# Optimization experiments

Measured on AMD Instinct MI355X. Metric: run time of the kernel, lower is better.

## Reference

```python
import jax, jax.numpy as jnp
import numpy as np

B, T, HID = 1, 2048, 1024
H, D = 16, 64
S = 64            # selection_block_size / sliding window / compress block
MAXK = 8          # max_selected_blocks
W_ENT, W_SP = 0.01, 0.01
NB = T // S       # 32 blocks (T divisible by S -> no padding branch)


def setup_inputs() -> dict:
    key = jax.random.key(0)
    ks = jax.random.split(key, 8)
    rn = lambda k, shp, s=0.02: jax.random.normal(k, shp, jnp.float32) * s
    return {
        'hidden_states': rn(ks[0], (B, T, HID), 1.0),
        'Wq': rn(ks[1], (HID, H * D)),
        'Wk': rn(ks[2], (HID, H * D)),
        'Wv': rn(ks[3], (HID, H * D)),
        'Wo': rn(ks[4], (H * D, HID)),
        'Wc': rn(ks[5], (S * D, D)),      # shared k/v compress MLP (same module in torch)
        'bc': jnp.zeros((D,), jnp.float32),
        'k_scale': jnp.ones((1,), jnp.float32),
        'k_bias': jnp.zeros((1,), jnp.float32),
        'Ws': rn(ks[6], (HID, 3 * H)),
        'bs': jnp.zeros((3 * H,), jnp.float32),
    }


def _local_attn(q, k, v):
    # lucidrains LocalAttention: window S, causal, look_backward=1, scale d^-0.5
    b, h, t, d = q.shape
    nw = t // S
    qw = q.reshape(b, h, nw, S, d)
    kw = k.reshape(b, h, nw, S, d)
    vw = v.reshape(b, h, nw, S, d)
    k_prev = jnp.concatenate([jnp.zeros_like(kw[:, :, :1]), kw[:, :, :-1]], axis=2)
    v_prev = jnp.concatenate([jnp.zeros_like(vw[:, :, :1]), vw[:, :, :-1]], axis=2)
    kc = jnp.concatenate([k_prev, kw], axis=3)   # (b,h,nw,2S,d)
    vc = jnp.concatenate([v_prev, vw], axis=3)
    scores = jnp.einsum('bhwid,bhwjd->bhwij', qw, kc) / jnp.sqrt(jnp.float32(d))
    qpos = jnp.arange(S)[:, None]
    krel = jnp.arange(2 * S)[None, :] - S        # key pos relative to window start
    wins = jnp.arange(nw)[:, None, None]
    allowed = (krel <= qpos)[None] & (wins * S + krel[None] >= 0)  # (nw,S,2S)
    NEG = -jnp.finfo(scores.dtype).max
    scores = jnp.where(allowed[None, None], scores, NEG)
    p = jax.nn.softmax(scores, axis=-1)
    return jnp.einsum('bhwij,bhwjd->bhwid', p, vc).reshape(b, h, t, d)


def reference(hidden_states, Wq, Wk, Wv, Wo, Wc, bc, k_scale, k_bias, Ws, bs):
    x = hidden_states
    scale = 1.0 / jnp.sqrt(jnp.float32(D))
    q = (x @ Wq).reshape(B, T, H, D).transpose(0, 2, 1, 3)
    k = (x @ Wk).reshape(B, T, H, D).transpose(0, 2, 1, 3)
    v = (x @ Wv).reshape(B, T, H, D).transpose(0, 2, 1, 3)

    sliding_out = _local_attn(q, k, v)

    # block compression (shared MLP for k and v, exact-erf GELU as in torch)
    k_blk = k.reshape(B, H, NB, S * D)
    v_blk = v.reshape(B, H, NB, S * D)
    kc = jax.nn.gelu(k_blk @ Wc + bc, approximate=False)   # (B,H,NB,D)
    vc = jax.nn.gelu(v_blk @ Wc + bc, approximate=False)

    importance = jnp.einsum('bhid,bhjd->bhij', q, kc) * scale   # (B,H,T,NB)
    comp_probs = jax.nn.softmax(importance, axis=-1)
    comp_out = jnp.einsum('bhij,bhjd->bhid', comp_probs, vc)

    # per-query-block scores, entropy-driven dynamic k
    block_scores = importance.reshape(B, H, NB, S, NB).mean(axis=3)   # (B,H,NB,NB)
    block_probs = jax.nn.softmax(block_scores, axis=-1)
    entropy = -jnp.sum(block_probs * jnp.log(block_probs + 1e-9), axis=-1)
    max_entropy = jnp.log(jnp.float32(NB))
    norm_ent = entropy / (max_entropy + 1e-9)
    k_ratio = jax.nn.sigmoid(k_scale[0] * norm_ent + k_bias[0])
    dynamic_k = jnp.clip(MAXK * k_ratio, 1.0, float(MAXK)).astype(jnp.int32)  # torch .long() truncates
    avg_k = dynamic_k.astype(jnp.float32).mean()

    _, topk_idx = jax.lax.top_k(block_scores, MAXK)                 # (B,H,NB,MAXK)
    k_mask = jnp.arange(MAXK)[None, None, None, :] < dynamic_k[..., None]
    sel = (topk_idx[..., None] == jnp.arange(NB)) & k_mask[..., None]
    mask = sel.any(axis=-2)                                         # (B,H,NB,NB)
    mask = mask | jnp.eye(NB, dtype=bool)[None, None]
    sparse_mask = jnp.repeat(jnp.repeat(mask, S, axis=2), S, axis=3)  # (B,H,T,T)

    attn = jnp.einsum('bhid,bhjd->bhij', q, k) * scale
    NEG = -jnp.finfo(attn.dtype).max
    attn = jnp.where(sparse_mask, attn, NEG)
    fine_probs = jax.nn.softmax(attn, axis=-1)
    fine_out = jnp.einsum('bhij,bhjd->bhid', fine_probs, v)

    strategy = jax.nn.sigmoid(x @ Ws + bs).reshape(B, T, H, 3).transpose(0, 2, 1, 3)  # (B,H,T,3)
    combined = jnp.stack([sliding_out, comp_out, fine_out], axis=-1)  # (B,H,T,D,3)
    out = jnp.einsum('bhnds,bhns->bhnd', combined, strategy)
    merged = out.transpose(0, 2, 1, 3).reshape(B, T, H * D)
    output = merged @ Wo

    entropy_loss = jnp.mean((k_ratio - norm_ent) ** 2)
    aux_loss = W_ENT * entropy_loss + W_SP * k_ratio.mean()
    return output, avg_k, aux_loss
```

## Files before the change

kernel.cpp:

```cpp
#include <hip/hip_runtime.h>
#include <math.h>
#include <stdint.h>

typedef unsigned short u16;
typedef short v8s __attribute__((ext_vector_type(8)));
typedef float v4f __attribute__((ext_vector_type(4)));

constexpr int kT   = 2048;
constexpr int kHID = 1024;
constexpr int kH   = 16;
constexpr int kNB  = 32;
constexpr size_t MB = 1ull << 20;

__device__ __forceinline__ float b2f(u16 u) { unsigned x = ((unsigned)u) << 16; return __uint_as_float(x); }
__device__ __forceinline__ u16 f2b(float f) {
  unsigned x = __float_as_uint(f);
  x += 0x7FFFu + ((x >> 16) & 1u);
  return (u16)(x >> 16);
}
__device__ __forceinline__ v4f mfma16(v8s a, v8s b, v4f c) {
  return __builtin_amdgcn_mfma_f32_16x16x32_bf16(a, b, c, 0, 0, 0);
}
__device__ __forceinline__ void gl_lds16(const void* g, void* l) {
  __builtin_amdgcn_global_load_lds((const __attribute__((address_space(1))) uint32_t*)g,
                                   (__attribute__((address_space(3))) uint32_t*)l, 16, 0, 0);
}

__global__ __launch_bounds__(256) void prep_kernel(
    const float* __restrict__ x, const float* __restrict__ Wq, const float* __restrict__ Wk,
    const float* __restrict__ Wv, const float* __restrict__ Wo, const float* __restrict__ Wc,
    const float* __restrict__ Wsp,
    u16* __restrict__ xh,
    u16* __restrict__ WqtH, u16* __restrict__ WktH,
    u16* __restrict__ WvtH, u16* __restrict__ WotH, u16* __restrict__ WctH, u16* __restrict__ WctL,
    u16* __restrict__ Wst) {
  __shared__ float tbuf[32][33];
  int bid = blockIdx.x;
  const int tid = threadIdx.x;
  if (bid < 1024) {
    int i = bid * 2048 + tid * 8;
    float4 a = *(const float4*)(x + i), b = *(const float4*)(x + i + 4);
    float tv[8] = {a.x, a.y, a.z, a.w, b.x, b.y, b.z, b.w};
    union { u16 s[8]; uint4 u; } hs;
#pragma unroll
    for (int e = 0; e < 8; ++e) hs.s[e] = f2b(tv[e]);
    *(uint4*)(xh + i) = hs.u;
    return;
  }
  bid -= 1024;
  const float* W; u16* Hh; u16* Ll; int Kd, Nd, bx, by;
  if (bid < 4096) {
    int wsel = bid >> 10, sub = bid & 1023;
    W  = wsel == 0 ? Wq : wsel == 1 ? Wk : wsel == 2 ? Wv : Wo;
    Hh = wsel == 0 ? WqtH : wsel == 1 ? WktH : wsel == 2 ? WvtH : WotH;
    Ll = nullptr;
    Kd = 1024; Nd = 1024;
    bx = (sub & 31) * 32; by = (sub >> 5) * 32;
  } else if (bid < 4096 + 256) {
    int sub = bid - 4096;
    W = Wc; Hh = WctH; Ll = WctL;
    Kd = 4096; Nd = 64;
    bx = (sub & 1) * 32; by = (sub >> 1) * 32;
  } else {
    int i = (bid - 4096 - 256) * 256 + tid;
    int n = i >> 10, k2 = i & 1023;
    float v = (n < 48) ? Wsp[(size_t)k2 * 48 + n] : 0.f;
    Wst[(size_t)n * 1024 + k2] = f2b(v);
    return;
  }
  const int lx = tid & 31, ly = tid >> 5;
  for (int i2 = ly; i2 < 32; i2 += 8) tbuf[i2][lx] = W[(size_t)(by + i2) * Nd + bx + lx];
  __syncthreads();
  for (int i2 = ly; i2 < 32; i2 += 8) {
    float xv = tbuf[lx][i2];
    size_t idx = (size_t)(bx + i2) * Kd + by + lx;
    u16 h = f2b(xv);
    Hh[idx] = h;
    if (Ll) Ll[idx] = f2b(xv - b2f(h));
  }
}

__global__ __launch_bounds__(256) void proj_gemm(const u16* __restrict__ xh,
                                                 const u16* __restrict__ WkH, const u16* __restrict__ WqH,
                                                 const u16* __restrict__ WvH, const u16* __restrict__ Wst,
                                                 const float* __restrict__ bsp,
                                                 u16* __restrict__ kbf, u16* __restrict__ qh,
                                                 u16* __restrict__ vbf, float* __restrict__ strat) {
  __shared__ u16 AsH[64 * 64], BsH[128 * 64];
  const int b = blockIdx.x;
  const int slot = (b & 7) * 100 + (b >> 3);
  const int panel = slot >> 5, bmi = slot & 31;
  int z, bni;
  if (panel < 8)       { z = 0; bni = panel; }
  else if (panel < 16) { z = 1; bni = panel - 8; }
  else if (panel < 24) { z = 2; bni = panel - 16; }
  else                 { z = 3; bni = 0; }
  const int bm = bmi * 64, bn = bni * 128;
  const u16* Bh = (z == 0) ? WkH : (z == 1) ? WqH : (z == 2) ? WvH : Wst;
  const int tid = threadIdx.x, w = tid >> 6, lane = tid & 63;
  const int lg = lane >> 4, l16 = lane & 15;
  const int wr = w >> 1, wc = w & 1;
  v4f acc[2][4] = {};
  for (int k0 = 0; k0 < kHID; k0 += 64) {
    __syncthreads();
#pragma unroll
    for (int p = 0; p < 2; ++p) {
      int s = tid + p * 256, row = s >> 3, sf = (s & 7) ^ (row & 7);
      gl_lds16(xh + (size_t)(bm + row) * kHID + k0 + sf * 8, (char*)AsH + s * 16);
    }
#pragma unroll
    for (int p = 0; p < 4; ++p) {
      int s = tid + p * 256, row = s >> 3, sf = (s & 7) ^ (row & 7);
      gl_lds16(Bh + (size_t)(bn + row) * kHID + k0 + sf * 8, (char*)BsH + s * 16);
    }
    __syncthreads();
#pragma unroll
    for (int kk = 0; kk < 2; ++kk) {
      v8s bh4[4];
#pragma unroll
      for (int j = 0; j < 4; ++j) {
        int col = wc * 64 + j * 16 + l16;
        bh4[j] = *(const v8s*)((const char*)BsH + col * 128 + (((kk * 4 + lg) ^ (col & 7)) * 16));
      }
#pragma unroll
      for (int i = 0; i < 2; ++i) {
        int row = wr * 32 + i * 16 + l16;
        v8s ah = *(const v8s*)((const char*)AsH + row * 128 + (((kk * 4 + lg) ^ (row & 7)) * 16));
#pragma unroll
        for (int j = 0; j < 4; ++j) acc[i][j] = mfma16(ah, bh4[j], acc[i][j]);
      }
    }
  }
#pragma unroll
  for (int i = 0; i < 2; ++i)
#pragma unroll
    for (int j = 0; j < 4; ++j)
#pragma unroll
      for (int r = 0; r < 4; ++r) {
        int row = bm + wr * 32 + i * 16 + lg * 4 + r;
        int col = bn + wc * 64 + j * 16 + l16;
        float val = acc[i][j][r];
        if (z == 3) {
          if (col < 48) strat[(size_t)row * 48 + col] = 1.f / (1.f + expf(-(val + bsp[col])));
        } else {
          u16 hh = f2b(val);
          size_t idx = (size_t)row * kHID + col;
          if (z == 0) kbf[idx] = hh;
          else if (z == 1) qh[idx] = hh;
          else vbf[idx] = hh;
        }
      }
}

__global__ __launch_bounds__(256) void cgemm_fused(const u16* __restrict__ kbf,
                                                   const u16* __restrict__ vbf,
                                                   const u16* __restrict__ WcH, const u16* __restrict__ WcL,
                                                   float* __restrict__ Pk, float* __restrict__ Pv) {
  __shared__ u16 AsH[64 * 64], BsH[64 * 64], BsL[64 * 64];
  const int bm = blockIdx.y * 64;
  const int isK = (blockIdx.z < 8);
  const int ks = isK ? blockIdx.z : blockIdx.z - 8;
  const u16* Asrc = isK ? kbf : vbf;
  float* P = isK ? Pk : Pv;
  const int tid = threadIdx.x;
  const int w = tid >> 6, lane = tid & 63;
  const int lg = lane >> 4, l16 = lane & 15;
  const int wr = w >> 1, wc = w & 1;
  v4f acc[2][2] = {};
  for (int k0 = ks * 512; k0 < ks * 512 + 512; k0 += 64) {
    __syncthreads();
#pragma unroll
    for (int ss = 0; ss < 2; ++ss) {
      int s = tid + ss * 256, row = s >> 3, sf = (s & 7) ^ (row & 7);
      int r = bm + row;
      size_t abase = ((size_t)((r & 31) * 64 + (k0 >> 6))) * kHID + (r >> 5) * 64 + sf * 8;
      gl_lds16(Asrc + abase, (char*)AsH + s * 16);
      gl_lds16(WcH + (size_t)row * 4096 + k0 + sf * 8, (char*)BsH + s * 16);
      if (isK) gl_lds16(WcL + (size_t)row * 4096 + k0 + sf * 8, (char*)BsL + s * 16);
    }
    __syncthreads();
    v8s ah[2][2], bh[2][2];
#pragma unroll
    for (int i = 0; i < 2; ++i)
#pragma unroll
      for (int kk = 0; kk < 2; ++kk) {
        int row = wr * 32 + i * 16 + l16;
        ah[i][kk] = *(const v8s*)((const char*)AsH + row * 128 + (((kk * 4 + lg) ^ (row & 7)) * 16));
        int col = wc * 32 + i * 16 + l16;
        bh[i][kk] = *(const v8s*)((const char*)BsH + col * 128 + (((kk * 4 + lg) ^ (col & 7)) * 16));
      }
#pragma unroll
    for (int i = 0; i < 2; ++i)
#pragma unroll
      for (int j = 0; j < 2; ++j) {
        acc[i][j] = mfma16(ah[i][0], bh[j][0], acc[i][j]);
        acc[i][j] = mfma16(ah[i][1], bh[j][1], acc[i][j]);
      }
    if (isK) {
      v8s bl[2][2];
#pragma unroll
      for (int i = 0; i < 2; ++i)
#pragma unroll
        for (int kk = 0; kk < 2; ++kk) {
          int col = wc * 32 + i * 16 + l16;
          bl[i][kk] = *(const v8s*)((const char*)BsL + col * 128 + (((kk * 4 + lg) ^ (col & 7)) * 16));
        }
#pragma unroll
      for (int i = 0; i < 2; ++i)
#pragma unroll
        for (int j = 0; j < 2; ++j) {
          acc[i][j] = mfma16(ah[i][0], bl[j][0], acc[i][j]);
          acc[i][j] = mfma16(ah[i][1], bl[j][1], acc[i][j]);
        }
    }
  }
#pragma unroll
  for (int i = 0; i < 2; ++i)
#pragma unroll
    for (int j = 0; j < 2; ++j)
#pragma unroll
      for (int r = 0; r < 4; ++r) {
        int row = bm + wr * 32 + i * 16 + lg * 4 + r;
        int col = wc * 32 + j * 16 + l16;
        P[(size_t)ks * 32768 + (size_t)row * 64 + col] = acc[i][j][r];
      }
}

__global__ __launch_bounds__(256) void attn_fused(const u16* __restrict__ qh,
                                                  const u16* __restrict__ kb_,
                                                  const u16* __restrict__ vb_,
                                                  const float* __restrict__ Pk,
                                                  const float* __restrict__ Pv,
                                                  const float* __restrict__ bc,
                                                  const float* __restrict__ strat,
                                                  const float* __restrict__ kscale_p,
                                                  const float* __restrict__ kbias_p,
                                                  float* __restrict__ krb,
                                                  float* __restrict__ neb,
                                                  int* __restrict__ dkb,
                                                  u16* __restrict__ merged) {
  __shared__ char smem[40960] __attribute__((aligned(128)));
  const int b = blockIdx.x;
  const int xcd = b & 7, slot = b >> 3;
  const int h = xcd + 8 * (slot >> 5);
  const int qb = slot & 31;
  const int tid = threadIdx.x, w = tid >> 6, lane = tid & 63;
  const int lg = lane >> 4, l16 = lane & 15;

  char* KCH = smem;
  char* KCL = smem + 4096;
  char* VCT = smem + 8192;
  u16*  PlA = (u16*)(smem + 12288);
  float* red = (float*)(smem + 16384);
  unsigned* mshare = (unsigned*)(smem + 16896);
  {
    int nb = tid >> 3, seg = tid & 7;
    {
      const float* base = Pk + ((size_t)(h * 32 + nb) * 64 + seg * 8);
      float v[8] = {};
#pragma unroll
      for (int ks = 0; ks < 8; ++ks) {
        const float* p = base + (size_t)ks * 32768;
        float4 a = *(const float4*)p, bq = *(const float4*)(p + 4);
        v[0] += a.x; v[1] += a.y; v[2] += a.z; v[3] += a.w;
        v[4] += bq.x; v[5] += bq.y; v[6] += bq.z; v[7] += bq.w;
      }
      v8s hi, lo;
#pragma unroll
      for (int e = 0; e < 8; ++e) {
        float s = v[e] + bc[seg * 8 + e];
        float g = 0.5f * s * (1.f + erff(s * 0.70710678118654752f));
        u16 hh = f2b(g);
        hi[e] = (short)hh;
        lo[e] = (short)f2b(g - b2f(hh));
      }
      *(v8s*)(KCH + nb * 128 + ((seg ^ (nb & 7)) * 16)) = hi;
      *(v8s*)(KCL + nb * 128 + ((seg ^ (nb & 7)) * 16)) = lo;
    }
    {
      const float* base = Pv + ((size_t)(h * 32 + nb) * 64 + seg * 8);
      float v[8] = {};
#pragma unroll
      for (int ks = 0; ks < 8; ++ks) {
        const float* p = base + (size_t)ks * 32768;
        float4 a = *(const float4*)p, bq = *(const float4*)(p + 4);
        v[0] += a.x; v[1] += a.y; v[2] += a.z; v[3] += a.w;
        v[4] += bq.x; v[5] += bq.y; v[6] += bq.z; v[7] += bq.w;
      }
#pragma unroll
      for (int e = 0; e < 8; ++e) {
        int d = seg * 8 + e;
        float s = v[e] + bc[d];
        float g = 0.5f * s * (1.f + erff(s * 0.70710678118654752f));
        *((u16*)(VCT + d * 64 + (((nb >> 3) ^ (d & 3)) * 16) + (nb & 7) * 2)) = f2b(g);
      }
    }
  }
  float st0r[4], st1r[4], st2r[4];
#pragma unroll
  for (int j = 0; j < 4; ++j) {
    int t = qb * 64 + w * 16 + lg * 4 + j;
    st0r[j] = strat[t * 48 + h * 3 + 0];
    st1r[j] = strat[t * 48 + h * 3 + 1];
    st2r[j] = strat[t * 48 + h * 3 + 2];
  }
  __syncthreads();
  const size_t qoff = (size_t)(qb * 64 + w * 16 + l16) * kHID + h * 64;
  v8s aq[2];
  aq[0] = *(const v8s*)(qh + qoff + lg * 8);
  aq[1] = *(const v8s*)(qh + qoff + 32 + lg * 8);
  v4f sa2[2] = {};
#pragma unroll
  for (int ct = 0; ct < 2; ++ct) {
    int col = ct * 16 + l16;
#pragma unroll
    for (int kk = 0; kk < 2; ++kk) {
      int bo = col * 128 + (((kk * 4 + lg) ^ (col & 7)) * 16);
      v8s bh = *(const v8s*)(KCH + bo);
      v8s bl = *(const v8s*)(KCL + bo);
      sa2[ct] = mfma16(aq[kk], bh, sa2[ct]);
      sa2[ct] = mfma16(aq[kk], bl, sa2[ct]);
    }
  }
#pragma unroll
  for (int ct = 0; ct < 2; ++ct)
#pragma unroll
    for (int j = 0; j < 4; ++j) sa2[ct][j] *= 0.125f;
#pragma unroll
  for (int ct = 0; ct < 2; ++ct) {
    float v = sa2[ct][0] + sa2[ct][1] + sa2[ct][2] + sa2[ct][3];
    v += __shfl_xor(v, 16, 64);
    v += __shfl_xor(v, 32, 64);
    if (lg == 0) red[w * 32 + ct * 16 + l16] = v;
  }
  float linv[4];
#pragma unroll
  for (int j = 0; j < 4; ++j) {
    float m = fmaxf(sa2[0][j], sa2[1][j]);
#pragma unroll
    for (int mm = 1; mm < 16; mm <<= 1) m = fmaxf(m, __shfl_xor(m, mm, 64));
    float e0 = __expf(sa2[0][j] - m), e1 = __expf(sa2[1][j] - m);
    float s = e0 + e1;
#pragma unroll
    for (int mm = 1; mm < 16; mm <<= 1) s += __shfl_xor(s, mm, 64);
    linv[j] = 1.f / s;
    int row = lg * 4 + j;
    PlA[w * 512 + row * 32 + l16] = f2b(e0);
    PlA[w * 512 + row * 32 + 16 + l16] = f2b(e1);
  }
  v8s pca = *(const v8s*)(PlA + w * 512 + l16 * 32 + lg * 8);
  float compC[4][4];
  {
    v4f o[4];
#pragma unroll
    for (int dt = 0; dt < 4; ++dt) {
      int d = dt * 16 + l16;
      v8s bb = *(const v8s*)(VCT + d * 64 + ((lg ^ (d & 3)) * 16));
      v4f z = {};
      o[dt] = mfma16(pca, bb, z);
#pragma unroll
      for (int j = 0; j < 4; ++j) compC[dt][j] = o[dt][j] * linv[j];
    }
  }
  __syncthreads();
  if (w == 0) {
    const int j = lane & 31;
    float bsj = (red[j] + red[32 + j] + red[64 + j] + red[96 + j]) * (1.f / 64.f);
    float mx = bsj;
#pragma unroll
    for (int m = 1; m < 32; m <<= 1) mx = fmaxf(mx, __shfl_xor(mx, m, 64));
    float e = expf(bsj - mx);
    float lsum = e;
#pragma unroll
    for (int m = 1; m < 32; m <<= 1) lsum += __shfl_xor(lsum, m, 64);
    float p = e / lsum;
    float ent = p * logf(p + 1e-9f);
#pragma unroll
    for (int m = 1; m < 32; m <<= 1) ent += __shfl_xor(ent, m, 64);
    ent = -ent;
    float ne = ent / (logf(32.f) + 1e-9f);
    float kr = 1.f / (1.f + expf(-(kscale_p[0] * ne + kbias_p[0])));
    int dk = (int)fminf(fmaxf(8.f * kr, 1.f), 8.f);
    unsigned mword = 1u << qb;
    int taken = 0;
    for (int r = 0; r < dk; ++r) {
      float v2 = taken ? -3.4e38f : bsj;
      int idx2 = j;
#pragma unroll
      for (int m = 1; m < 32; m <<= 1) {
        float ov = __shfl_xor(v2, m, 64);
        int oi = __shfl_xor(idx2, m, 64);
        if (ov > v2 || (ov == v2 && oi < idx2)) { v2 = ov; idx2 = oi; }
      }
      mword |= (1u << idx2);
      if (j == idx2) taken = 1;
    }
    if (lane == 0) {
      krb[h * kNB + qb] = kr;
      neb[h * kNB + qb] = ne;
      dkb[h * kNB + qb] = dk;
      *mshare = mword;
    }
  }
  __syncthreads();
  const unsigned mword = *mshare;
  __syncthreads();

  char* KbB = smem;
  char* VtB = smem + 16384;
  char* PlB = smem + 32768;
  unsigned uni = mword | (1u << qb);
  if (qb > 0) uni |= 1u << (qb - 1);
  float mF[4], lF[4], mS[4], lS[4];
  v4f oF[4] = {}, oS[4] = {};
#pragma unroll
  for (int j = 0; j < 4; ++j) { mF[j] = -1e30f; lF[j] = 0.f; mS[j] = -1e30f; lS[j] = 0.f; }
  const int vkey = tid & 63, vd0 = (tid >> 6) * 16;

  auto k_stage = [&](int buf, int jb) {
#pragma unroll
    for (int ss = 0; ss < 2; ++ss) {
      int s = tid + ss * 256;
      int key = s >> 3, sf = (s & 7) ^ (key & 7);
      gl_lds16(kb_ + (size_t)(jb * 64 + key) * kHID + h * 64 + sf * 8, KbB + buf * 8192 + s * 16);
    }
  };
  auto v_issue = [&](int jb, uint4& c0, uint4& c1) {
    const u16* vsrc = vb_ + (size_t)(jb * 64 + vkey) * kHID + h * 64 + vd0;
    c0 = *(const uint4*)(vsrc);
    c1 = *(const uint4*)(vsrc + 8);
  };
  auto v_write = [&](int buf, uint4 c0, uint4 c1) {
    union { uint4 u[2]; u16 s[16]; } c;
    c.u[0] = c0; c.u[1] = c1;
#pragma unroll
    for (int i = 0; i < 16; ++i) {
      int d = vd0 + i;
      *((u16*)(VtB + buf * 8192 + d * 128 + (((vkey >> 3) ^ (d & 7)) * 16)) + (vkey & 7)) = c.s[i];
    }
  };
  auto upd = [&](const v4f* sa, float* m_run, float* l_run, v4f* o_acc, int buf) {
    float corr[4];
#pragma unroll
    for (int j = 0; j < 4; ++j) {
      float t = fmaxf(fmaxf(sa[0][j], sa[1][j]), fmaxf(sa[2][j], sa[3][j]));
#pragma unroll
      for (int mm = 1; mm < 16; mm <<= 1) t = fmaxf(t, __shfl_xor(t, mm, 64));
      float mn = fmaxf(m_run[j], t);
      corr[j] = __expf(m_run[j] - mn);
      m_run[j] = mn;
    }
    float rs[4] = {0.f, 0.f, 0.f, 0.f};
    float pv[4][4];
#pragma unroll
    for (int ct = 0; ct < 4; ++ct)
#pragma unroll
      for (int j = 0; j < 4; ++j) {
        float e = __expf(sa[ct][j] - m_run[j]);
        pv[ct][j] = e;
        rs[j] += e;
      }
#pragma unroll
    for (int j = 0; j < 4; ++j) {
#pragma unroll
      for (int mm = 1; mm < 16; mm <<= 1) rs[j] += __shfl_xor(rs[j], mm, 64);
      l_run[j] = l_run[j] * corr[j] + rs[j];
    }
#pragma unroll
    for (int ct = 0; ct < 4; ++ct)
#pragma unroll
      for (int j = 0; j < 4; ++j) {
        int row = lg * 4 + j;
        int seg = ct * 2 + (l16 >> 3);
        *((u16*)(PlB + w * 2048 + row * 128 + ((seg ^ (row & 7)) * 16)) + (l16 & 7)) = f2b(pv[ct][j]);
      }
#pragma unroll
    for (int dt = 0; dt < 4; ++dt)
#pragma unroll
      for (int j = 0; j < 4; ++j) o_acc[dt][j] *= corr[j];
    __builtin_amdgcn_s_setprio(1);
#pragma unroll
    for (int dt = 0; dt < 4; ++dt) {
      int d = dt * 16 + l16;
#pragma unroll
      for (int kk = 0; kk < 2; ++kk) {
        v8s pa = *(const v8s*)(PlB + w * 2048 + l16 * 128 + (((kk * 4 + lg) ^ (l16 & 7)) * 16));
        v8s vb2 = *(const v8s*)(VtB + buf * 8192 + d * 128 + (((kk * 4 + lg) ^ (d & 7)) * 16));
        o_acc[dt] = mfma16(pa, vb2, o_acc[dt]);
      }
    }
    __builtin_amdgcn_s_setprio(0);
  };

  int jb_cur = __builtin_ctz(uni);
  unsigned rem = uni & (uni - 1);
  uint4 vc0, vc1;
  v_issue(jb_cur, vc0, vc1);
  k_stage(0, jb_cur);
  v_write(0, vc0, vc1);
  int buf = 0;
  while (jb_cur >= 0) {
    int jb_next = -1;
    if (rem) { jb_next = __builtin_ctz(rem); rem &= rem - 1; }
    __syncthreads();
    if (jb_next >= 0) { v_issue(jb_next, vc0, vc1); k_stage(buf ^ 1, jb_next); }
    v4f sa[4] = {};
    __builtin_amdgcn_s_setprio(1);
#pragma unroll
    for (int ct = 0; ct < 4; ++ct) {
      int key = ct * 16 + l16;
#pragma unroll
      for (int kk = 0; kk < 2; ++kk) {
        v8s bk = *(const v8s*)(KbB + buf * 8192 + key * 128 + (((kk * 4 + lg) ^ (key & 7)) * 16));
        sa[ct] = mfma16(aq[kk], bk, sa[ct]);
      }
    }
    __builtin_amdgcn_s_setprio(0);
#pragma unroll
    for (int ct = 0; ct < 4; ++ct)
#pragma unroll
      for (int j = 0; j < 4; ++j) sa[ct][j] *= 0.125f;
    const bool inF = (mword >> jb_cur) & 1u;
    const bool inS = (jb_cur == qb) || (jb_cur + 1 == qb);
    if (inF) upd(sa, mF, lF, oF, buf);
    if (inS) {
      v4f sb[4];
#pragma unroll
      for (int ct = 0; ct < 4; ++ct) sb[ct] = sa[ct];
      if (jb_cur == qb) {
#pragma unroll
        for (int ct = 0; ct < 4; ++ct) {
          int key = ct * 16 + l16;
#pragma unroll
          for (int j = 0; j < 4; ++j) {
            int qp = w * 16 + lg * 4 + j;
            if (key > qp) sb[ct][j] = -1e30f;
          }
        }
      }
      upd(sb, mS, lS, oS, buf);
    }
    if (jb_next >= 0) v_write(buf ^ 1, vc0, vc1);
    jb_cur = jb_next;
    buf ^= 1;
  }
#pragma unroll
  for (int j = 0; j < 4; ++j) {
    int t = qb * 64 + w * 16 + lg * 4 + j;
    float invS = 1.f / lS[j], invF = 1.f / lF[j];
#pragma unroll
    for (int dt = 0; dt < 4; ++dt) {
      int d = dt * 16 + l16;
      size_t idx = (size_t)t * kHID + h * 64 + d;
      float val = st0r[j] * (oS[dt][j] * invS) + st1r[j] * compC[dt][j] + st2r[j] * (oF[dt][j] * invF);
      merged[idx] = f2b(val);
    }
  }
}

__global__ __launch_bounds__(256) void gemm_out(const u16* __restrict__ A, const u16* __restrict__ Bt,
                                                const float* __restrict__ krb, const float* __restrict__ neb,
                                                const int* __restrict__ dkb, float* __restrict__ Cf) {
  __shared__ u16 As[64 * 64], Bs[64 * 64];
  const int b = blockIdx.x;
  const int g = (b & 7) * 64 + (b >> 3);
  const int bn = (g >> 5) * 64;
  const int bm = (g & 31) * 64;
  const int tid = threadIdx.x, w = tid >> 6, lane = tid & 63;
  const int lg = lane >> 4, l16 = lane & 15;
  if (b == 0 && w == 3) {
    float s1 = 0.f, s2 = 0.f, s3 = 0.f;
    for (int i = lane; i < 512; i += 64) {
      float fdk = (float)dkb[i], kr = krb[i], ne = neb[i];
      float d2 = kr - ne;
      s1 += fdk; s2 += d2 * d2; s3 += kr;
    }
#pragma unroll
    for (int m = 1; m < 64; m <<= 1) {
      s1 += __shfl_xor(s1, m, 64);
      s2 += __shfl_xor(s2, m, 64);
      s3 += __shfl_xor(s3, m, 64);
    }
    if (lane == 0) {
      Cf[(size_t)kT * kHID + 0] = s1 * (1.f / 512.f);
      Cf[(size_t)kT * kHID + 1] = 0.01f * (s2 * (1.f / 512.f)) + 0.01f * (s3 * (1.f / 512.f));
    }
  }
  v4f acc[4] = {};
  for (int k0 = 0; k0 < kHID; k0 += 64) {
    __syncthreads();
#pragma unroll
    for (int p = 0; p < 2; ++p) {
      int s = tid + p * 256, row = s >> 3, sf = (s & 7) ^ (row & 7);
      gl_lds16(A + (size_t)(bm + row) * kHID + k0 + sf * 8, (char*)As + s * 16);
      gl_lds16(Bt + (size_t)(bn + row) * kHID + k0 + sf * 8, (char*)Bs + s * 16);
    }
    __syncthreads();
#pragma unroll
    for (int kk = 0; kk < 2; ++kk) {
      int row = w * 16 + l16;
      v8s a = *(const v8s*)((const char*)As + row * 128 + (((kk * 4 + lg) ^ (row & 7)) * 16));
#pragma unroll
      for (int j = 0; j < 4; ++j) {
        int col = j * 16 + l16;
        v8s bb = *(const v8s*)((const char*)Bs + col * 128 + (((kk * 4 + lg) ^ (col & 7)) * 16));
        acc[j] = mfma16(a, bb, acc[j]);
      }
    }
  }
#pragma unroll
  for (int j = 0; j < 4; ++j)
#pragma unroll
    for (int r = 0; r < 4; ++r) {
      int row = bm + w * 16 + lg * 4 + r;
      int col = bn + j * 16 + l16;
      Cf[(size_t)row * kHID + col] = acc[j][r];
    }
}

extern "C" void kernel_launch(void* const* d_in, const int* in_sizes, int n_in,
                              void* d_out, int out_size, void* d_ws, size_t ws_size,
                              hipStream_t stream) {
  const float* x      = (const float*)d_in[0];
  const float* Wq     = (const float*)d_in[1];
  const float* Wk     = (const float*)d_in[2];
  const float* Wv     = (const float*)d_in[3];
  const float* Wo     = (const float*)d_in[4];
  const float* Wc     = (const float*)d_in[5];
  const float* bc     = (const float*)d_in[6];
  const float* kscale = (const float*)d_in[7];
  const float* kbias  = (const float*)d_in[8];
  const float* Wsp    = (const float*)d_in[9];
  const float* bsp    = (const float*)d_in[10];
  float* out = (float*)d_out;
  char* W = (char*)d_ws;

  u16* qh     = (u16*)(W + 0 * MB);
  u16* kbf    = (u16*)(W + 8 * MB);
  u16* vbf    = (u16*)(W + 16 * MB);
  u16* merged = (u16*)(W + 20 * MB);
  u16* xh     = (u16*)(W + 24 * MB);
  u16* WqtH   = (u16*)(W + 32 * MB);
  u16* WktH   = (u16*)(W + 36 * MB);
  u16* WvtH   = (u16*)(W + 40 * MB);
  u16* WotH   = (u16*)(W + 42 * MB);
  u16* WctH   = (u16*)(W + 44 * MB);
  u16* WctL   = (u16*)(W + 44 * MB + 512 * 1024);
  u16* Wst    = (u16*)(W + 45 * MB);
  float* strat= (float*)(W + 46 * MB);
  float* Pk   = (float*)(W + 47 * MB);
  float* Pv   = (float*)(W + 48 * MB);
  float* krb  = (float*)(W + 49 * MB + 4 * 1024);
  float* neb  = (float*)(W + 49 * MB + 8 * 1024);
  int*   dkb  = (int*)(W + 49 * MB + 12 * 1024);

  dim3 b256(256);
  prep_kernel<<<5888, b256, 0, stream>>>(x, Wq, Wk, Wv, Wo, Wc, Wsp,
                                         xh, WqtH, WktH, WvtH, WotH, WctH, WctL, Wst);
  proj_gemm<<<800, b256, 0, stream>>>(xh, WktH, WqtH, WvtH, Wst,
                                      bsp, kbf, qh, vbf, strat);
  cgemm_fused<<<dim3(1, 8, 16), b256, 0, stream>>>(kbf, vbf, WctH, WctL, Pk, Pv);
  attn_fused<<<512, b256, 0, stream>>>(qh, kbf, vbf, Pk, Pv, bc, strat,
                                       kscale, kbias, krb, neb, dkb, merged);
  gemm_out<<<512, b256, 0, stream>>>(merged, WotH, krb, neb, dkb, out);
}
```

Before: 89.04 us.

## Drop split-bf16 Wc low part and prefetch diagonal K/V block early in attention

Removes the bf16 hi/lo split of the compress weight for the K path, so cgemm runs a single bf16 product and prep no longer writes the low-part array. In attn_fused, the diagonal block's K/V staging is issued at kernel start so it overlaps the compression/selection phase. The LDS layout is reorganised to make room, and the shared buffer grows to 51200 bytes. The s_setprio hints are removed. Dropping the low-part correction lowers the precision of compressed keys, which could change which blocks get selected.

```diff
diff --git a/kernel.cpp b/kernel.cpp
--- a/kernel.cpp
+++ b/kernel.cpp
@@ -32,7 +32,7 @@
     const float* __restrict__ Wsp,
     u16* __restrict__ xh,
     u16* __restrict__ WqtH, u16* __restrict__ WktH,
-    u16* __restrict__ WvtH, u16* __restrict__ WotH, u16* __restrict__ WctH, u16* __restrict__ WctL,
+    u16* __restrict__ WvtH, u16* __restrict__ WotH, u16* __restrict__ WctH,
     u16* __restrict__ Wst) {
   __shared__ float tbuf[32][33];
   int bid = blockIdx.x;
@@ -48,17 +48,16 @@
     return;
   }
   bid -= 1024;
-  const float* W; u16* Hh; u16* Ll; int Kd, Nd, bx, by;
+  const float* W; u16* Hh; int Kd, Nd, bx, by;
   if (bid < 4096) {
     int wsel = bid >> 10, sub = bid & 1023;
     W  = wsel == 0 ? Wq : wsel == 1 ? Wk : wsel == 2 ? Wv : Wo;
     Hh = wsel == 0 ? WqtH : wsel == 1 ? WktH : wsel == 2 ? WvtH : WotH;
-    Ll = nullptr;
     Kd = 1024; Nd = 1024;
     bx = (sub & 31) * 32; by = (sub >> 5) * 32;
   } else if (bid < 4096 + 256) {
     int sub = bid - 4096;
-    W = Wc; Hh = WctH; Ll = WctL;
+    W = Wc; Hh = WctH;
     Kd = 4096; Nd = 64;
     bx = (sub & 1) * 32; by = (sub >> 1) * 32;
   } else {
@@ -73,10 +72,7 @@
   __syncthreads();
   for (int i2 = ly; i2 < 32; i2 += 8) {
     float xv = tbuf[lx][i2];
-    size_t idx = (size_t)(bx + i2) * Kd + by + lx;
-    u16 h = f2b(xv);
-    Hh[idx] = h;
-    if (Ll) Ll[idx] = f2b(xv - b2f(h));
+    Hh[(size_t)(bx + i2) * Kd + by + lx] = f2b(xv);
   }
 }
 
@@ -154,9 +150,9 @@
 
 __global__ __launch_bounds__(256) void cgemm_fused(const u16* __restrict__ kbf,
                                                    const u16* __restrict__ vbf,
-                                                   const u16* __restrict__ WcH, const u16* __restrict__ WcL,
+                                                   const u16* __restrict__ WcH,
                                                    float* __restrict__ Pk, float* __restrict__ Pv) {
-  __shared__ u16 AsH[64 * 64], BsH[64 * 64], BsL[64 * 64];
+  __shared__ u16 AsH[64 * 64], BsH[64 * 64];
   const int bm = blockIdx.y * 64;
   const int isK = (blockIdx.z < 8);
   const int ks = isK ? blockIdx.z : blockIdx.z - 8;
@@ -176,7 +172,6 @@
       size_t abase = ((size_t)((r & 31) * 64 + (k0 >> 6))) * kHID + (r >> 5) * 64 + sf * 8;
       gl_lds16(Asrc + abase, (char*)AsH + s * 16);
       gl_lds16(WcH + (size_t)row * 4096 + k0 + sf * 8, (char*)BsH + s * 16);
-      if (isK) gl_lds16(WcL + (size_t)row * 4096 + k0 + sf * 8, (char*)BsL + s * 16);
     }
     __syncthreads();
     v8s ah[2][2], bh[2][2];
@@ -196,23 +191,6 @@
         acc[i][j] = mfma16(ah[i][0], bh[j][0], acc[i][j]);
         acc[i][j] = mfma16(ah[i][1], bh[j][1], acc[i][j]);
       }
-    if (isK) {
-      v8s bl[2][2];
-#pragma unroll
-      for (int i = 0; i < 2; ++i)
-#pragma unroll
-        for (int kk = 0; kk < 2; ++kk) {
-          int col = wc * 32 + i * 16 + l16;
-          bl[i][kk] = *(const v8s*)((const char*)BsL + col * 128 + (((kk * 4 + lg) ^ (col & 7)) * 16));
-        }
-#pragma unroll
-      for (int i = 0; i < 2; ++i)
-#pragma unroll
-        for (int j = 0; j < 2; ++j) {
-          acc[i][j] = mfma16(ah[i][0], bl[j][0], acc[i][j]);
-          acc[i][j] = mfma16(ah[i][1], bl[j][1], acc[i][j]);
-        }
-    }
   }
 #pragma unroll
   for (int i = 0; i < 2; ++i)
@@ -239,7 +217,7 @@
                                                   float* __restrict__ neb,
                                                   int* __restrict__ dkb,
                                                   u16* __restrict__ merged) {
-  __shared__ char smem[40960] __attribute__((aligned(128)));
+  __shared__ char smem[51200] __attribute__((aligned(128)));
   const int b = blockIdx.x;
   const int xcd = b & 7, slot = b >> 3;
   const int h = xcd + 8 * (slot >> 5);
@@ -253,6 +231,38 @@
   u16*  PlA = (u16*)(smem + 12288);
   float* red = (float*)(smem + 16384);
   unsigned* mshare = (unsigned*)(smem + 16896);
+  char* PlB = smem;
+  char* KbB = smem + 18432;
+  char* VtB = smem + 34816;
+
+  const int vkey = tid & 63, vd0 = (tid >> 6) * 16;
+  auto k_stage = [&](int buf, int jb) {
+#pragma unroll
+    for (int ss = 0; ss < 2; ++ss) {
+      int s = tid + ss * 256;
+      int key = s >> 3, sf = (s & 7) ^ (key & 7);
+      gl_lds16(kb_ + (size_t)(jb * 64 + key) * kHID + h * 64 + sf * 8, KbB + buf * 8192 + s * 16);
+    }
+  };
+  auto v_issue = [&](int jb, uint4& c0, uint4& c1) {
+    const u16* vsrc = vb_ + (size_t)(jb * 64 + vkey) * kHID + h * 64 + vd0;
+    c0 = *(const uint4*)(vsrc);
+    c1 = *(const uint4*)(vsrc + 8);
+  };
+  auto v_write = [&](int buf, uint4 c0, uint4 c1) {
+    union { uint4 u[2]; u16 s[16]; } c;
+    c.u[0] = c0; c.u[1] = c1;
+#pragma unroll
+    for (int i = 0; i < 16; ++i) {
+      int d = vd0 + i;
+      *((u16*)(VtB + buf * 8192 + d * 128 + (((vkey >> 3) ^ (d & 7)) * 16)) + (vkey & 7)) = c.s[i];
+    }
+  };
+
+  uint4 vc0, vc1;
+  k_stage(0, qb);
+  v_issue(qb, vc0, vc1);
+
   {
     int nb = tid >> 3, seg = tid & 7;
     {
@@ -362,6 +372,7 @@
       for (int j = 0; j < 4; ++j) compC[dt][j] = o[dt][j] * linv[j];
     }
   }
+  v_write(0, vc0, vc1);
   __syncthreads();
   if (w == 0) {
     const int j = lane & 31;
@@ -406,39 +417,13 @@
   const unsigned mword = *mshare;
   __syncthreads();
 
-  char* KbB = smem;
-  char* VtB = smem + 16384;
-  char* PlB = smem + 32768;
   unsigned uni = mword | (1u << qb);
   if (qb > 0) uni |= 1u << (qb - 1);
   float mF[4], lF[4], mS[4], lS[4];
   v4f oF[4] = {}, oS[4] = {};
 #pragma unroll
   for (int j = 0; j < 4; ++j) { mF[j] = -1e30f; lF[j] = 0.f; mS[j] = -1e30f; lS[j] = 0.f; }
-  const int vkey = tid & 63, vd0 = (tid >> 6) * 16;
-
-  auto k_stage = [&](int buf, int jb) {
-#pragma unroll
-    for (int ss = 0; ss < 2; ++ss) {
-      int s = tid + ss * 256;
-      int key = s >> 3, sf = (s & 7) ^ (key & 7);
-      gl_lds16(kb_ + (size_t)(jb * 64 + key) * kHID + h * 64 + sf * 8, KbB + buf * 8192 + s * 16);
-    }
-  };
-  auto v_issue = [&](int jb, uint4& c0, uint4& c1) {
-    const u16* vsrc = vb_ + (size_t)(jb * 64 + vkey) * kHID + h * 64 + vd0;
-    c0 = *(const uint4*)(vsrc);
-    c1 = *(const uint4*)(vsrc + 8);
-  };
-  auto v_write = [&](int buf, uint4 c0, uint4 c1) {
-    union { uint4 u[2]; u16 s[16]; } c;
-    c.u[0] = c0; c.u[1] = c1;
-#pragma unroll
-    for (int i = 0; i < 16; ++i) {
-      int d = vd0 + i;
-      *((u16*)(VtB + buf * 8192 + d * 128 + (((vkey >> 3) ^ (d & 7)) * 16)) + (vkey & 7)) = c.s[i];
-    }
-  };
+
   auto upd = [&](const v4f* sa, float* m_run, float* l_run, v4f* o_acc, int buf) {
     float corr[4];
 #pragma unroll
@@ -478,7 +463,6 @@
     for (int dt = 0; dt < 4; ++dt)
 #pragma unroll
       for (int j = 0; j < 4; ++j) o_acc[dt][j] *= corr[j];
-    __builtin_amdgcn_s_setprio(1);
 #pragma unroll
     for (int dt = 0; dt < 4; ++dt) {
       int d = dt * 16 + l16;
@@ -489,15 +473,10 @@
         o_acc[dt] = mfma16(pa, vb2, o_acc[dt]);
       }
     }
-    __builtin_amdgcn_s_setprio(0);
   };
 
-  int jb_cur = __builtin_ctz(uni);
-  unsigned rem = uni & (uni - 1);
-  uint4 vc0, vc1;
-  v_issue(jb_cur, vc0, vc1);
-  k_stage(0, jb_cur);
-  v_write(0, vc0, vc1);
+  int jb_cur = qb;
+  unsigned rem = uni & ~(1u << qb);
   int buf = 0;
   while (jb_cur >= 0) {
     int jb_next = -1;
@@ -505,7 +484,6 @@
     __syncthreads();
     if (jb_next >= 0) { v_issue(jb_next, vc0, vc1); k_stage(buf ^ 1, jb_next); }
     v4f sa[4] = {};
-    __builtin_amdgcn_s_setprio(1);
 #pragma unroll
     for (int ct = 0; ct < 4; ++ct) {
       int key = ct * 16 + l16;
@@ -515,7 +493,6 @@
         sa[ct] = mfma16(aq[kk], bk, sa[ct]);
       }
     }
-    __builtin_amdgcn_s_setprio(0);
 #pragma unroll
     for (int ct = 0; ct < 4; ++ct)
 #pragma unroll
@@ -645,7 +622,6 @@
   u16* WvtH   = (u16*)(W + 40 * MB);
   u16* WotH   = (u16*)(W + 42 * MB);
   u16* WctH   = (u16*)(W + 44 * MB);
-  u16* WctL   = (u16*)(W + 44 * MB + 512 * 1024);
   u16* Wst    = (u16*)(W + 45 * MB);
   float* strat= (float*)(W + 46 * MB);
   float* Pk   = (float*)(W + 47 * MB);
@@ -656,10 +632,10 @@
 
   dim3 b256(256);
   prep_kernel<<<5888, b256, 0, stream>>>(x, Wq, Wk, Wv, Wo, Wc, Wsp,
-                                         xh, WqtH, WktH, WvtH, WotH, WctH, WctL, Wst);
+                                         xh, WqtH, WktH, WvtH, WotH, WctH, Wst);
   proj_gemm<<<800, b256, 0, stream>>>(xh, WktH, WqtH, WvtH, Wst,
                                       bsp, kbf, qh, vbf, strat);
-  cgemm_fused<<<dim3(1, 8, 16), b256, 0, stream>>>(kbf, vbf, WctH, WctL, Pk, Pv);
+  cgemm_fused<<<dim3(1, 8, 16), b256, 0, stream>>>(kbf, vbf, WctH, Pk, Pv);
   attn_fused<<<512, b256, 0, stream>>>(qh, kbf, vbf, Pk, Pv, bc, strat,
                                        kscale, kbias, krb, neb, dkb, merged);
   gemm_out<<<512, b256, 0, stream>>>(merged, WotH, krb, neb, dkb, out);
```

Measured after the change: 88.38 us. Within noise of the previous version (-0.7%).
